# Kernel tuning notes

Measured on AMD Instinct MI355X. Metric: run time of the kernel, lower is better.

## Reference

```python
import jax, jax.numpy as jnp
import numpy as np

TOP_K = 4
N_GROUP = 4
TOPK_GROUP = 2
ROUTED_SCALING = 1.0


def setup_inputs() -> dict:
    key = jax.random.key(0)
    k1, k2, k3, k4, k5 = jax.random.split(key, 5)
    B, S, H, I, E = 1, 2048, 1024, 512, 16
    hidden_states = jax.random.normal(k1, (B, S, H), dtype=jnp.float32)
    # router weight (kaiming-uniform-like scale)
    gate_weight = jax.random.normal(k2, (E, H), dtype=jnp.float32) * (1.0 / np.sqrt(H))
    e_bias = jnp.zeros((E,), dtype=jnp.float32)  # e_score_correction_bias buffer
    gate_proj = jax.random.normal(k3, (E, I, H), dtype=jnp.float32) * 0.02
    up_proj = jax.random.normal(k4, (E, I, H), dtype=jnp.float32) * 0.02
    down_proj = jax.random.normal(k5, (E, H, I), dtype=jnp.float32) * 0.02
    return {
        "hidden_states": hidden_states,
        "gate_weight": gate_weight,
        "e_bias": e_bias,
        "gate_proj": gate_proj,
        "up_proj": up_proj,
        "down_proj": down_proj,
    }


def _route(x_flat, gate_weight, e_bias):
    # x_flat: [T, H]
    T = x_flat.shape[0]
    E = gate_weight.shape[0]
    logits = jnp.einsum("th,eh->te", x_flat, gate_weight)
    scores = jax.nn.sigmoid(logits)                      # [T, E]
    scores_for_choice = scores + e_bias[None, :]
    # group scores = sum of top-2 expert scores within each group
    grp = scores_for_choice.reshape(T, N_GROUP, E // N_GROUP)
    top2, _ = jax.lax.top_k(grp, 2)
    group_scores = top2.sum(axis=-1)                     # [T, G]
    _, group_idx = jax.lax.top_k(group_scores, TOPK_GROUP)
    group_mask = jax.nn.one_hot(group_idx, N_GROUP, dtype=scores.dtype).sum(axis=1)  # [T, G]
    score_mask = jnp.repeat(group_mask, E // N_GROUP, axis=1)                        # [T, E]
    tmp_scores = jnp.where(score_mask > 0, scores_for_choice, 0.0)
    _, topk_idx = jax.lax.top_k(tmp_scores, TOP_K)       # [T, K]
    topk_weight = jnp.take_along_axis(scores, topk_idx, axis=1)
    denom = topk_weight.sum(axis=-1, keepdims=True) + 1e-20
    topk_weight = topk_weight / denom * ROUTED_SCALING
    return topk_idx, topk_weight


def reference(hidden_states, gate_weight, e_bias, gate_proj, up_proj, down_proj):
    B, S, H = hidden_states.shape
    E = gate_proj.shape[0]
    x = hidden_states.reshape(-1, H).astype(jnp.float32)  # [T, H]
    topk_idx, topk_weight = _route(x, gate_weight, e_bias)
    # combine weights per (token, expert): sum over the k slots selecting e
    combine = (jax.nn.one_hot(topk_idx, E, dtype=x.dtype) * topk_weight[..., None]).sum(axis=1)  # [T, E]
    # dense expert MLP (mathematically equal to gather-compute-scatter since
    # non-selected experts receive zero combine weight)
    g = jnp.einsum("th,eih->tei", x, gate_proj)
    u = jnp.einsum("th,eih->tei", x, up_proj)
    act = jax.nn.silu(g) * u                              # [T, E, I]
    expert_out = jnp.einsum("tei,ehi->teh", act, down_proj)
    y = jnp.einsum("teh,te->th", expert_out, combine)
    return y.reshape(B, S, H)
```

## Files before the change

### kernel.cpp

```cpp
#include <hip/hip_runtime.h>
#include <hip/hip_bf16.h>

typedef __attribute__((ext_vector_type(8))) short bf16x8;
typedef __attribute__((ext_vector_type(4))) float f32x4;

#define T_TOK 2048
#define HD 1024
#define ID 512
#define NE 16
#define TOPK 4
#define BK 64
#define WELEM (HD*ID*NE)

__device__ __forceinline__ unsigned pk2(float a, float b) {
    return __builtin_amdgcn_perm(__float_as_uint(b), __float_as_uint(a),
                                 0x07060302u);
}
__device__ __forceinline__ bf16x8 cvt8(const float* __restrict__ p) {
    float4 a = *(const float4*)p;
    float4 b = *(const float4*)(p + 4);
    union { bf16x8 v; unsigned u[4]; } r;
    r.u[0] = pk2(a.x, a.y); r.u[1] = pk2(a.z, a.w);
    r.u[2] = pk2(b.x, b.y); r.u[3] = pk2(b.z, b.w);
    return r.v;
}
__device__ __forceinline__ short f2bf(float f) {
    unsigned u = __float_as_uint(f);
    return (short)((u + 0x7fffu + ((u >> 16) & 1u)) >> 16);
}
__device__ __forceinline__ float bf2f(short s) {
    return __uint_as_float(((unsigned)(unsigned short)s) << 16);
}
__device__ __forceinline__ void load_lds16(const short* g, short* l) {
    __builtin_amdgcn_global_load_lds(
        (const __attribute__((address_space(1))) unsigned*)g,
        (__attribute__((address_space(3))) unsigned*)l, 16, 0, 0);
}

#define MFMA_BF16 __builtin_amdgcn_mfma_f32_16x16x32_bf16

__global__ __launch_bounds__(256) void conv_k(
        const float* __restrict__ s0, short* __restrict__ d0,
        const float* __restrict__ s1, short* __restrict__ d1,
        const float* __restrict__ s2, short* __restrict__ d2) {
    const float* src = (blockIdx.y == 0) ? s0 : (blockIdx.y == 1) ? s1 : s2;
    short* dst       = (blockIdx.y == 0) ? d0 : (blockIdx.y == 1) ? d1 : d2;
    size_t i = ((size_t)blockIdx.x * 256 + threadIdx.x) * 8;
    union { bf16x8 v; uint4 q; } r;
    r.v = cvt8(src + i);
    *(uint4*)(dst + i) = r.q;
}

__global__ __launch_bounds__(256) void router_k(
        const float* __restrict__ x, const float* __restrict__ gw,
        const float* __restrict__ eb,
        int* __restrict__ tk_idx, float* __restrict__ tk_w,
        short* __restrict__ xb) {
    int wid  = (blockIdx.x * 256 + threadIdx.x) >> 6;
    int lane = threadIdx.x & 63;

    const float* xr = x + (size_t)wid * HD + lane * 16;
    float xv[16];
#pragma unroll
    for (int c = 0; c < 4; c++) {
        float4 v = *(const float4*)(xr + c * 4);
        xv[4 * c] = v.x; xv[4 * c + 1] = v.y; xv[4 * c + 2] = v.z; xv[4 * c + 3] = v.w;
    }
    {
        union { uint4 q; unsigned u[4]; } w0, w1;
        w0.u[0] = pk2(xv[0], xv[1]);  w0.u[1] = pk2(xv[2], xv[3]);
        w0.u[2] = pk2(xv[4], xv[5]);  w0.u[3] = pk2(xv[6], xv[7]);
        w1.u[0] = pk2(xv[8], xv[9]);  w1.u[1] = pk2(xv[10], xv[11]);
        w1.u[2] = pk2(xv[12], xv[13]); w1.u[3] = pk2(xv[14], xv[15]);
        short* d = xb + ((size_t)wid << 10) + lane * 16;
        *(uint4*)d = w0.q;
        *(uint4*)(d + 8) = w1.q;
    }

    float logits[NE];
#pragma unroll
    for (int e = 0; e < NE; e++) {
        const float* gr = gw + e * HD + lane * 16;
        float p = 0.f;
#pragma unroll
        for (int c = 0; c < 4; c++) {
            float4 v = *(const float4*)(gr + c * 4);
            p += xv[4 * c] * v.x + xv[4 * c + 1] * v.y +
                 xv[4 * c + 2] * v.z + xv[4 * c + 3] * v.w;
        }
#pragma unroll
        for (int s = 32; s > 0; s >>= 1) p += __shfl_xor(p, s, 64);
        logits[e] = p;
    }

    float scores[NE], sc[NE];
#pragma unroll
    for (int e = 0; e < NE; e++) {
        scores[e] = 1.f / (1.f + __expf(-logits[e]));
        sc[e] = scores[e] + eb[e];
    }

    float gs[4];
#pragma unroll
    for (int g = 0; g < 4; g++) {
        float a = sc[4 * g], b = sc[4 * g + 1], c = sc[4 * g + 2], d = sc[4 * g + 3];
        float h1 = fmaxf(a, b), l1 = fminf(a, b);
        float h2 = fmaxf(c, d), l2 = fminf(c, d);
        gs[g] = fmaxf(h1, h2) + fmaxf(fminf(h1, h2), fmaxf(l1, l2));
    }
    int g0 = 0; float b0 = gs[0];
#pragma unroll
    for (int g = 1; g < 4; g++) if (gs[g] > b0) { b0 = gs[g]; g0 = g; }
    int g1 = -1; float b1 = -1e30f;
#pragma unroll
    for (int g = 0; g < 4; g++) if (g != g0 && gs[g] > b1) { b1 = gs[g]; g1 = g; }

    int taken = 0;
    int bid[TOPK]; float bsc[TOPK]; float wsum = 0.f;
#pragma unroll
    for (int k = 0; k < TOPK; k++) {
        float bv = -1e30f; int bi = 0; float bs = 0.f;
#pragma unroll
        for (int e = 0; e < NE; e++) {
            int grp = e >> 2;
            bool ok = ((grp == g0) || (grp == g1)) && !((taken >> e) & 1);
            if (ok && sc[e] > bv) { bv = sc[e]; bi = e; bs = scores[e]; }
        }
        taken |= (1 << bi);
        bid[k] = bi; bsc[k] = bs; wsum += bs;
    }
    if (lane == 0) {
        float inv = 1.0f / (wsum + 1e-20f);
#pragma unroll
        for (int k = 0; k < TOPK; k++) {
            tk_idx[wid * TOPK + k] = bid[k];
            tk_w[wid * TOPK + k]   = bsc[k] * inv;
        }
    }
}

__global__ __launch_bounds__(256) void assign_k(
        const int* __restrict__ tk_idx,
        int* __restrict__ counts, int* __restrict__ tok_list,
        int* __restrict__ pair_slot) {
    int p = blockIdx.x * 256 + threadIdx.x;
    int e = tk_idx[p];
    int slot = atomicAdd(&counts[e], 1);
    tok_list[e * T_TOK + slot] = p >> 2;
    pair_slot[p] = slot;
}

__global__ void offs_k(const int* __restrict__ counts, int* __restrict__ offs) {
    if (threadIdx.x == 0) {
        int a = 0;
#pragma unroll
        for (int e = 0; e < NE; e++) { offs[e] = a; a += counts[e]; }
    }
}

__global__ __launch_bounds__(256) void gemm1_k(
        const short* __restrict__ xb,
        const short* __restrict__ gpb,
        const short* __restrict__ upb,
        const int* __restrict__ counts,
        const int* __restrict__ offs,
        const int* __restrict__ tok_list,
        short* __restrict__ act) {
    __shared__ short xs[128 * BK];
    __shared__ short gs[64 * BK];
    __shared__ short us[64 * BK];
    __shared__ int   tok_s[128];

    int e = blockIdx.z;
    int cnt = counts[e];
    int base = blockIdx.y * 128;
    if (base >= cnt) return;
    int arow0 = offs[e] + base;

    int tid = threadIdx.x;
    if (tid < 128) {
        int s = base + tid;
        tok_s[tid] = (s < cnt) ? tok_list[e * T_TOK + s] : tok_list[e * T_TOK];
    }
    __syncthreads();

    int wv = tid >> 6, lane = tid & 63;
    int qd = lane >> 4, l16 = lane & 15;
    int wm = (wv >> 1) * 64, wn = (wv & 1) * 32;
    int nb0 = blockIdx.x * 64;
    const short* gp = gpb + (size_t)e * ID * HD + (size_t)nb0 * HD;
    const short* up = upb + (size_t)e * ID * HD + (size_t)nb0 * HD;

    const short* xsg[4]; short* xld[4];
#pragma unroll
    for (int i = 0; i < 4; i++) {
        int idx = i * 256 + tid, r = idx >> 3, c = idx & 7;
        xsg[i] = xb + ((size_t)tok_s[r] << 10) + (((c ^ r) & 7) << 3);
        xld[i] = &xs[(i * 256 + wv * 64) * 8];
    }
    const short* gsg[2]; const short* usg[2]; short* gld[2]; short* uld[2];
#pragma unroll
    for (int i = 0; i < 2; i++) {
        int idx = i * 256 + tid, r = idx >> 3, c = idx & 7;
        size_t so = (size_t)r * HD + (((c ^ r) & 7) << 3);
        gsg[i] = gp + so;
        usg[i] = up + so;
        gld[i] = &gs[(i * 256 + wv * 64) * 8];
        uld[i] = &us[(i * 256 + wv * 64) * 8];
    }

    f32x4 accg[4][2] = {};
    f32x4 accu[4][2] = {};

    for (int kp = 0; kp < HD; kp += BK) {
#pragma unroll
        for (int i = 0; i < 4; i++) load_lds16(xsg[i] + kp, xld[i]);
#pragma unroll
        for (int i = 0; i < 2; i++) {
            load_lds16(gsg[i] + kp, gld[i]);
            load_lds16(usg[i] + kp, uld[i]);
        }
        __syncthreads();
#pragma unroll
        for (int ks = 0; ks < 2; ks++) {
            int cb = ks * 4 + qd;
            bf16x8 af[4], bg[2], bu[2];
#pragma unroll
            for (int i = 0; i < 4; i++) {
                int r = wm + i * 16 + l16;
                af[i] = *(const bf16x8*)&xs[(r << 6) + (((cb ^ r) & 7) << 3)];
            }
#pragma unroll
            for (int j = 0; j < 2; j++) {
                int r = wn + j * 16 + l16;
                int lo = (r << 6) + (((cb ^ r) & 7) << 3);
                bg[j] = *(const bf16x8*)&gs[lo];
                bu[j] = *(const bf16x8*)&us[lo];
            }
#pragma unroll
            for (int i = 0; i < 4; i++)
#pragma unroll
                for (int j = 0; j < 2; j++) {
                    accg[i][j] = MFMA_BF16(af[i], bg[j], accg[i][j], 0, 0, 0);
                    accu[i][j] = MFMA_BF16(af[i], bu[j], accu[i][j], 0, 0, 0);
                }
        }
        __syncthreads();
    }

#pragma unroll
    for (int i = 0; i < 4; i++)
#pragma unroll
        for (int j = 0; j < 2; j++)
#pragma unroll
            for (int r = 0; r < 4; r++) {
                int m = wm + i * 16 + qd * 4 + r;
                if (base + m < cnt) {
                    float g = accg[i][j][r], u = accu[i][j][r];
                    float a = g / (1.f + __expf(-g)) * u;
                    act[(size_t)(arow0 + m) * ID + nb0 + wn + j * 16 + l16] = f2bf(a);
                }
            }
}

__global__ __launch_bounds__(256) void gemm2_k(
        const short* __restrict__ act,
        const short* __restrict__ dpb,
        const int* __restrict__ counts,
        const int* __restrict__ offs,
        short* __restrict__ yexp) {
    __shared__ short as_[128 * BK];
    __shared__ short ds_[128 * BK];

    int e = blockIdx.z;
    int cnt = counts[e];
    int base = blockIdx.y * 128;
    if (base >= cnt) return;
    int arow0 = offs[e] + base;

    int tid = threadIdx.x;
    int wv = tid >> 6, lane = tid & 63;
    int qd = lane >> 4, l16 = lane & 15;
    int wm = (wv >> 1) * 64, wn = (wv & 1) * 64;
    int hb0 = blockIdx.x * 128;
    const short* dp = dpb + (size_t)e * HD * ID + (size_t)hb0 * ID;

    const short* asg[4]; const short* dsg[4]; short* ald[4]; short* dld[4];
#pragma unroll
    for (int i = 0; i < 4; i++) {
        int idx = i * 256 + tid, r = idx >> 3, c = idx & 7;
        int sw = ((c ^ r) & 7) << 3;
        asg[i] = act + (size_t)(arow0 + r) * ID + sw;
        dsg[i] = dp + (size_t)r * ID + sw;
        ald[i] = &as_[(i * 256 + wv * 64) * 8];
        dld[i] = &ds_[(i * 256 + wv * 64) * 8];
    }

    f32x4 acc[4][4] = {};

    for (int kp = 0; kp < ID; kp += BK) {
#pragma unroll
        for (int i = 0; i < 4; i++) {
            load_lds16(asg[i] + kp, ald[i]);
            load_lds16(dsg[i] + kp, dld[i]);
        }
        __syncthreads();
#pragma unroll
        for (int ks = 0; ks < 2; ks++) {
            int cb = ks * 4 + qd;
            bf16x8 af[4], bd[4];
#pragma unroll
            for (int i = 0; i < 4; i++) {
                int r = wm + i * 16 + l16;
                af[i] = *(const bf16x8*)&as_[(r << 6) + (((cb ^ r) & 7) << 3)];
                int r2 = wn + i * 16 + l16;
                bd[i] = *(const bf16x8*)&ds_[(r2 << 6) + (((cb ^ r2) & 7) << 3)];
            }
#pragma unroll
            for (int i = 0; i < 4; i++)
#pragma unroll
                for (int j = 0; j < 4; j++)
                    acc[i][j] = MFMA_BF16(af[i], bd[j], acc[i][j], 0, 0, 0);
        }
        __syncthreads();
    }

#pragma unroll
    for (int i = 0; i < 4; i++)
#pragma unroll
        for (int j = 0; j < 4; j++)
#pragma unroll
            for (int r = 0; r < 4; r++) {
                int m = wm + i * 16 + qd * 4 + r;
                if (base + m < cnt)
                    yexp[(size_t)(arow0 + m) * HD + hb0 + wn + j * 16 + l16] =
                        f2bf(acc[i][j][r]);
            }
}

__global__ __launch_bounds__(256) void combine_k(
        const short* __restrict__ yexp,
        const int* __restrict__ offs,
        const int* __restrict__ tk_idx, const float* __restrict__ tk_w,
        const int* __restrict__ pair_slot,
        float* __restrict__ out) {
    int t = blockIdx.x * 2 + (threadIdx.x >> 7);
    int i = threadIdx.x & 127;
    float acc[8] = {};
#pragma unroll
    for (int k = 0; k < TOPK; k++) {
        int p = t * TOPK + k;
        int e = tk_idx[p];
        int row = offs[e] + pair_slot[p];
        float w = tk_w[p];
        bf16x8 v = *(const bf16x8*)(yexp + (size_t)row * HD + i * 8);
#pragma unroll
        for (int j = 0; j < 8; j++) acc[j] += w * bf2f(v[j]);
    }
    float4 o0 = {acc[0], acc[1], acc[2], acc[3]};
    float4 o1 = {acc[4], acc[5], acc[6], acc[7]};
    float* d = out + (size_t)t * HD + i * 8;
    *(float4*)d = o0;
    *(float4*)(d + 4) = o1;
}

extern "C" void kernel_launch(void* const* d_in, const int* in_sizes, int n_in,
                              void* d_out, int out_size, void* d_ws, size_t ws_size,
                              hipStream_t stream) {
    const float* x  = (const float*)d_in[0];
    const float* gw = (const float*)d_in[1];
    const float* eb = (const float*)d_in[2];
    const float* gp = (const float*)d_in[3];
    const float* up = (const float*)d_in[4];
    const float* dp = (const float*)d_in[5];

    short* gpb = (short*)d_ws;
    short* upb = gpb + WELEM;
    short* dpb = upb + WELEM;
    short* xb  = dpb + WELEM;
    short* act = xb + (size_t)T_TOK * HD;
    int* counts    = (int*)(act + (size_t)(T_TOK * TOPK + 128) * ID);
    int* offs      = counts + NE;
    int* tok_list  = offs + NE;
    int* pair_slot = tok_list + NE * T_TOK;
    int* tk_idx    = pair_slot + T_TOK * TOPK;
    float* tk_w    = (float*)(tk_idx + T_TOK * TOPK);
    short* yexp = gpb;

    hipMemsetAsync(counts, 0, NE * sizeof(int), stream);

    conv_k<<<dim3(WELEM / 8 / 256, 3), 256, 0, stream>>>(gp, gpb, up, upb,
                                                         dp, dpb);
    router_k<<<T_TOK / 4, 256, 0, stream>>>(x, gw, eb, tk_idx, tk_w, xb);
    assign_k<<<T_TOK * TOPK / 256, 256, 0, stream>>>(tk_idx, counts,
                                                     tok_list, pair_slot);
    offs_k<<<1, 64, 0, stream>>>(counts, offs);
    gemm1_k<<<dim3(ID / 64, T_TOK / 128, NE), 256, 0, stream>>>(
        xb, gpb, upb, counts, offs, tok_list, act);
    gemm2_k<<<dim3(HD / 128, T_TOK / 128, NE), 256, 0, stream>>>(
        act, dpb, counts, offs, yexp);
    combine_k<<<T_TOK / 2, 256, 0, stream>>>(yexp, offs, tk_idx, tk_w,
                                             pair_slot, (float*)d_out);
}
```

Measured before the change: 245.3 us.

## Double-buffer LDS tiles in both expert GEMMs to overlap loads with MFMA

```diff
diff --git a/kernel.cpp b/kernel.cpp
--- a/kernel.cpp
+++ b/kernel.cpp
@@ -166,9 +166,9 @@
         const int* __restrict__ offs,
         const int* __restrict__ tok_list,
         short* __restrict__ act) {
-    __shared__ short xs[128 * BK];
-    __shared__ short gs[64 * BK];
-    __shared__ short us[64 * BK];
+    __shared__ short xs[2][128 * BK];
+    __shared__ short gs[2][64 * BK];
+    __shared__ short us[2][64 * BK];
     __shared__ int   tok_s[128];
 
     int e = blockIdx.z;
@@ -196,7 +196,7 @@
     for (int i = 0; i < 4; i++) {
         int idx = i * 256 + tid, r = idx >> 3, c = idx & 7;
         xsg[i] = xb + ((size_t)tok_s[r] << 10) + (((c ^ r) & 7) << 3);
-        xld[i] = &xs[(i * 256 + wv * 64) * 8];
+        xld[i] = &xs[0][(i * 256 + wv * 64) * 8];
     }
     const short* gsg[2]; const short* usg[2]; short* gld[2]; short* uld[2];
 #pragma unroll
@@ -205,22 +205,27 @@
         size_t so = (size_t)r * HD + (((c ^ r) & 7) << 3);
         gsg[i] = gp + so;
         usg[i] = up + so;
-        gld[i] = &gs[(i * 256 + wv * 64) * 8];
-        uld[i] = &us[(i * 256 + wv * 64) * 8];
+        gld[i] = &gs[0][(i * 256 + wv * 64) * 8];
+        uld[i] = &us[0][(i * 256 + wv * 64) * 8];
     }
 
     f32x4 accg[4][2] = {};
     f32x4 accu[4][2] = {};
 
-    for (int kp = 0; kp < HD; kp += BK) {
-#pragma unroll
-        for (int i = 0; i < 4; i++) load_lds16(xsg[i] + kp, xld[i]);
+    auto STAGE = [&](int kp, int b) {
+#pragma unroll
+        for (int i = 0; i < 4; i++)
+            load_lds16(xsg[i] + kp, xld[i] + b * (128 * BK));
 #pragma unroll
         for (int i = 0; i < 2; i++) {
-            load_lds16(gsg[i] + kp, gld[i]);
-            load_lds16(usg[i] + kp, uld[i]);
-        }
-        __syncthreads();
+            load_lds16(gsg[i] + kp, gld[i] + b * (64 * BK));
+            load_lds16(usg[i] + kp, uld[i] + b * (64 * BK));
+        }
+    };
+    auto COMPUTE = [&](int b) {
+        const short* xsb = xs[b];
+        const short* gsb = gs[b];
+        const short* usb = us[b];
 #pragma unroll
         for (int ks = 0; ks < 2; ks++) {
             int cb = ks * 4 + qd;
@@ -228,14 +233,14 @@
 #pragma unroll
             for (int i = 0; i < 4; i++) {
                 int r = wm + i * 16 + l16;
-                af[i] = *(const bf16x8*)&xs[(r << 6) + (((cb ^ r) & 7) << 3)];
+                af[i] = *(const bf16x8*)&xsb[(r << 6) + (((cb ^ r) & 7) << 3)];
             }
 #pragma unroll
             for (int j = 0; j < 2; j++) {
                 int r = wn + j * 16 + l16;
                 int lo = (r << 6) + (((cb ^ r) & 7) << 3);
-                bg[j] = *(const bf16x8*)&gs[lo];
-                bu[j] = *(const bf16x8*)&us[lo];
+                bg[j] = *(const bf16x8*)&gsb[lo];
+                bu[j] = *(const bf16x8*)&usb[lo];
             }
 #pragma unroll
             for (int i = 0; i < 4; i++)
@@ -245,8 +250,25 @@
                     accu[i][j] = MFMA_BF16(af[i], bu[j], accu[i][j], 0, 0, 0);
                 }
         }
-        __syncthreads();
-    }
+    };
+
+    constexpr int NP = HD / BK;
+    STAGE(0, 0);
+    auto STEP = [&](int p, int b) {
+        if (p + 1 < NP) {
+            STAGE((p + 1) * BK, b ^ 1);
+            asm volatile("s_waitcnt vmcnt(8)" ::: "memory");
+        } else {
+            asm volatile("s_waitcnt vmcnt(0)" ::: "memory");
+        }
+        __builtin_amdgcn_s_barrier();
+        asm volatile("" ::: "memory");
+        COMPUTE(b);
+        asm volatile("" ::: "memory");
+        __builtin_amdgcn_s_barrier();
+    };
+#pragma unroll 1
+    for (int p = 0; p < NP; p += 2) { STEP(p, 0); STEP(p + 1, 1); }
 
 #pragma unroll
     for (int i = 0; i < 4; i++)
@@ -269,8 +291,8 @@
         const int* __restrict__ counts,
         const int* __restrict__ offs,
         short* __restrict__ yexp) {
-    __shared__ short as_[128 * BK];
-    __shared__ short ds_[128 * BK];
+    __shared__ short as_[2][128 * BK];
+    __shared__ short ds_[2][128 * BK];
 
     int e = blockIdx.z;
     int cnt = counts[e];
@@ -292,19 +314,22 @@
         int sw = ((c ^ r) & 7) << 3;
         asg[i] = act + (size_t)(arow0 + r) * ID + sw;
         dsg[i] = dp + (size_t)r * ID + sw;
-        ald[i] = &as_[(i * 256 + wv * 64) * 8];
-        dld[i] = &ds_[(i * 256 + wv * 64) * 8];
+        ald[i] = &as_[0][(i * 256 + wv * 64) * 8];
+        dld[i] = &ds_[0][(i * 256 + wv * 64) * 8];
     }
 
     f32x4 acc[4][4] = {};
 
-    for (int kp = 0; kp < ID; kp += BK) {
+    auto STAGE = [&](int kp, int b) {
 #pragma unroll
         for (int i = 0; i < 4; i++) {
-            load_lds16(asg[i] + kp, ald[i]);
-            load_lds16(dsg[i] + kp, dld[i]);
-        }
-        __syncthreads();
+            load_lds16(asg[i] + kp, ald[i] + b * (128 * BK));
+            load_lds16(dsg[i] + kp, dld[i] + b * (128 * BK));
+        }
+    };
+    auto COMPUTE = [&](int b) {
+        const short* asb = as_[b];
+        const short* dsb = ds_[b];
 #pragma unroll
         for (int ks = 0; ks < 2; ks++) {
             int cb = ks * 4 + qd;
@@ -312,9 +337,9 @@
 #pragma unroll
             for (int i = 0; i < 4; i++) {
                 int r = wm + i * 16 + l16;
-                af[i] = *(const bf16x8*)&as_[(r << 6) + (((cb ^ r) & 7) << 3)];
+                af[i] = *(const bf16x8*)&asb[(r << 6) + (((cb ^ r) & 7) << 3)];
                 int r2 = wn + i * 16 + l16;
-                bd[i] = *(const bf16x8*)&ds_[(r2 << 6) + (((cb ^ r2) & 7) << 3)];
+                bd[i] = *(const bf16x8*)&dsb[(r2 << 6) + (((cb ^ r2) & 7) << 3)];
             }
 #pragma unroll
             for (int i = 0; i < 4; i++)
@@ -322,8 +347,25 @@
                 for (int j = 0; j < 4; j++)
                     acc[i][j] = MFMA_BF16(af[i], bd[j], acc[i][j], 0, 0, 0);
         }
-        __syncthreads();
-    }
+    };
+
+    constexpr int NP = ID / BK;
+    STAGE(0, 0);
+    auto STEP = [&](int p, int b) {
+        if (p + 1 < NP) {
+            STAGE((p + 1) * BK, b ^ 1);
+            asm volatile("s_waitcnt vmcnt(8)" ::: "memory");
+        } else {
+            asm volatile("s_waitcnt vmcnt(0)" ::: "memory");
+        }
+        __builtin_amdgcn_s_barrier();
+        asm volatile("" ::: "memory");
+        COMPUTE(b);
+        asm volatile("" ::: "memory");
+        __builtin_amdgcn_s_barrier();
+    };
+#pragma unroll 1
+    for (int p = 0; p < NP; p += 2) { STEP(p, 0); STEP(p + 1, 1); }
 
 #pragma unroll
     for (int i = 0; i < 4; i++)
```

Result: no change. 246.3 us (+0.4%).
